# Optimization experiments

Hardware: AMD Instinct MI355X
Metric: run time of the kernel (lower is better)

Reference implementation:

```python
import jax, jax.numpy as jnp
import numpy as np

B, T, C = 8, 2048, 1024
NEG_INF = -1e38


def setup_inputs() -> dict:
    key = jax.random.key(0)
    ks = jax.random.split(key, 10)
    s = 1.0 / np.sqrt(C)
    return {
        "x": jax.random.normal(ks[0], (B, T, C), jnp.float32),
        "Wk": jax.random.normal(ks[1], (C, C), jnp.float32) * s,
        "Wv": jax.random.normal(ks[2], (C, C), jnp.float32) * s,
        "Wr": jax.random.normal(ks[3], (C, C), jnp.float32) * s,
        "Wo": jax.random.normal(ks[4], (C, C), jnp.float32) * s,
        "time_decay": jax.random.normal(ks[5], (C,), jnp.float32) * 0.5,
        "time_first": jax.random.normal(ks[6], (C,), jnp.float32) * 0.5,
        "time_mix_key": jax.random.uniform(ks[7], (1, 1, C), jnp.float32),
        "time_mix_value": jax.random.uniform(ks[8], (1, 1, C), jnp.float32),
        "time_mix_receptance": jax.random.uniform(ks[9], (1, 1, C), jnp.float32),
    }


def _wkv(k, v, time_decay, time_first):
    # k, v: [B, T, C]; numerically-stabilized exp-sum recurrence over T
    w = -jnp.exp(time_decay)  # [C]
    u = time_first            # [C]

    def step(carry, kv):
        num, den, mx = carry
        kt, vt = kv  # [B, C]
        # output at this step uses u bonus
        m_out = jnp.maximum(mx, kt + u)
        e1 = jnp.exp(mx - m_out)
        e2 = jnp.exp(kt + u - m_out)
        out = (e1 * num + e2 * vt) / (e1 * den + e2)
        # state update with decay w
        m_new = jnp.maximum(mx + w, kt)
        e1 = jnp.exp(mx + w - m_new)
        e2 = jnp.exp(kt - m_new)
        return (e1 * num + e2 * vt, e1 * den + e2, m_new), out

    init = (jnp.zeros((B, C), jnp.float32),
            jnp.zeros((B, C), jnp.float32),
            jnp.full((B, C), NEG_INF, jnp.float32))
    kT = jnp.swapaxes(k, 0, 1)  # [T, B, C]
    vT = jnp.swapaxes(v, 0, 1)
    _, outs = jax.lax.scan(step, init, (kT, vT))
    return jnp.swapaxes(outs, 0, 1)  # [B, T, C]


def reference(x, Wk, Wv, Wr, Wo, time_decay, time_first,
              time_mix_key, time_mix_value, time_mix_receptance):
    # time_shift: prev_x[t] = x[t-1], zero at t=0
    prev_x = jnp.concatenate([jnp.zeros_like(x[:, :1]), x[:, :-1]], axis=1)

    r_in = x * time_mix_receptance + prev_x * (1 - time_mix_receptance)
    k_in = x * time_mix_key + prev_x * (1 - time_mix_key)
    v_in = x * time_mix_value + prev_x * (1 - time_mix_value)

    receptance = jnp.einsum('btc,dc->btd', r_in, Wr)
    key = jnp.einsum('btc,dc->btd', k_in, Wk)
    value = jnp.einsum('btc,dc->btd', v_in, Wv)

    wkv = _wkv(key, value, time_decay, time_first)
    rwkv = jax.nn.sigmoid(receptance) * wkv
    return jnp.einsum('btc,dc->btd', rwkv, Wo)
```

## Files before the change

### kernel.cpp

```cpp
#include <hip/hip_runtime.h>
#include <cstdint>
#include <cstddef>

#define DEVI __device__ __forceinline__

typedef __attribute__((ext_vector_type(8))) short short8;
typedef __attribute__((ext_vector_type(4))) float f32x4;

constexpr int Bc = 8, Tc = 2048, Cc = 1024;
constexpr int WKV_L = 32, WKV_NCH = 64;

DEVI unsigned short f2b(float f) {
  unsigned int u = __float_as_uint(f);
  unsigned int r = (u + 0x7FFFu + ((u >> 16) & 1u)) >> 16;
  return (unsigned short)r;
}
DEVI float b2f(unsigned short u) {
  return __uint_as_float(((unsigned int)u) << 16);
}

DEVI void gload16(const unsigned short* g, unsigned short* l) {
  __builtin_amdgcn_global_load_lds(
      (const __attribute__((address_space(1))) void*)g,
      (__attribute__((address_space(3))) void*)l, 16, 0, 0);
}

__global__ void convert_bf16_kernel(const float* __restrict__ in,
                                    unsigned short* __restrict__ out, int n4) {
  int i = blockIdx.x * blockDim.x + threadIdx.x;
  if (i >= n4) return;
  const float4 v = ((const float4*)in)[i];
  ushort4 o;
  o.x = f2b(v.x); o.y = f2b(v.y); o.z = f2b(v.z); o.w = f2b(v.w);
  ((ushort4*)out)[i] = o;
}

__global__ void mix3_kernel(const float* __restrict__ x,
                            const float* __restrict__ tmk,
                            const float* __restrict__ tmv,
                            const float* __restrict__ tmr,
                            unsigned short* __restrict__ kin,
                            unsigned short* __restrict__ vin,
                            unsigned short* __restrict__ rin,
                            long n4) {
  long i = (long)blockIdx.x * blockDim.x + threadIdx.x;
  const long stride = (long)gridDim.x * blockDim.x;
  for (; i < n4; i += stride) {
    const long e = i * 4;
    const int c = (int)(e & (Cc - 1));
    const long bt = e >> 10;
    const int t = (int)(bt & (Tc - 1));
    const float4 xv = *(const float4*)(x + e);
    float4 pv = {0.f, 0.f, 0.f, 0.f};
    if (t > 0) pv = *(const float4*)(x + e - Cc);
    const float4 mk = *(const float4*)(tmk + c);
    const float4 mv = *(const float4*)(tmv + c);
    const float4 mr = *(const float4*)(tmr + c);
    const float* xp = (const float*)&xv;
    const float* pp = (const float*)&pv;
    const float* mkp = (const float*)&mk;
    const float* mvp = (const float*)&mv;
    const float* mrp = (const float*)&mr;
    ushort4 ko, vo, ro;
    unsigned short* kop = (unsigned short*)&ko;
    unsigned short* vop = (unsigned short*)&vo;
    unsigned short* rop = (unsigned short*)&ro;
#pragma unroll
    for (int q = 0; q < 4; ++q) {
      kop[q] = f2b(xp[q] * mkp[q] + pp[q] * (1.f - mkp[q]));
      vop[q] = f2b(xp[q] * mvp[q] + pp[q] * (1.f - mvp[q]));
      rop[q] = f2b(xp[q] * mrp[q] + pp[q] * (1.f - mrp[q]));
    }
    *(ushort4*)(kin + e) = ko;
    *(ushort4*)(vin + e) = vo;
    *(ushort4*)(rin + e) = ro;
  }
}

template <typename OutT>
__global__ __launch_bounds__(512, 2)
void gemm256(const unsigned short* __restrict__ A0,
             const unsigned short* __restrict__ W0, OutT* __restrict__ C0,
             const unsigned short* __restrict__ A1,
             const unsigned short* __restrict__ W1, OutT* __restrict__ C1,
             const unsigned short* __restrict__ A2,
             const unsigned short* __restrict__ W2, OutT* __restrict__ C2,
             int K, int N) {
  constexpr int BK = 64;
  __shared__ alignas(16) unsigned short As[2][256 * BK];
  __shared__ alignas(16) unsigned short Bs[2][256 * BK];
  const int z = blockIdx.z;
  const unsigned short* A = z == 0 ? A0 : (z == 1 ? A1 : A2);
  const unsigned short* W = z == 0 ? W0 : (z == 1 ? W1 : W2);
  OutT* C_out = z == 0 ? C0 : (z == 1 ? C1 : C2);
  const int m0 = blockIdx.x * 256;
  const int n0 = blockIdx.y * 256;
  const int tid = threadIdx.x;
  const int lane = tid & 63;
  const int w = tid >> 6;
  const int wm = w >> 2;
  const int wn = w & 3;
  const int fr = lane & 15;
  const int ksl = lane >> 4;

  f32x4 acc[8][4];
#pragma unroll
  for (int i = 0; i < 8; ++i)
#pragma unroll
    for (int j = 0; j < 4; ++j) acc[i][j] = (f32x4){0.f, 0.f, 0.f, 0.f};

#define STAGE(buf, kt)                                                        \
  {                                                                           \
    _Pragma("unroll")                                                         \
    for (int cc = 0; cc < 4; ++cc) {                                          \
      const int c = w * 256 + cc * 64 + lane;                                 \
      const int row = c >> 3;                                                 \
      const int gsl = (c & 7) ^ (row & 7);                                    \
      gload16(A + (size_t)(m0 + row) * K + (kt) + gsl * 8,                    \
              &As[buf][(w * 256 + cc * 64) * 8]);                             \
      gload16(W + (size_t)(n0 + row) * K + (kt) + gsl * 8,                    \
              &Bs[buf][(w * 256 + cc * 64) * 8]);                             \
    }                                                                         \
  }

  const int nt = K / BK;
  STAGE(0, 0);
  int cur = 0;
  for (int t = 0; t < nt; ++t) {
    asm volatile("s_waitcnt vmcnt(0)" ::: "memory");
    __builtin_amdgcn_s_barrier();
    asm volatile("" ::: "memory");
    if (t + 1 < nt) STAGE(cur ^ 1, (t + 1) * BK);
#pragma unroll
    for (int ks = 0; ks < 2; ++ks) {
      const int sl = ks * 4 + ksl;
      short8 af[8], bf[4];
#pragma unroll
      for (int i = 0; i < 8; ++i) {
        const int row = wm * 128 + i * 16 + fr;
        af[i] = *(const short8*)&As[cur][row * 64 + ((sl ^ (row & 7)) * 8)];
      }
#pragma unroll
      for (int j = 0; j < 4; ++j) {
        const int row = wn * 64 + j * 16 + fr;
        bf[j] = *(const short8*)&Bs[cur][row * 64 + ((sl ^ (row & 7)) * 8)];
      }
      __builtin_amdgcn_s_setprio(1);
#pragma unroll
      for (int i = 0; i < 8; ++i)
#pragma unroll
        for (int j = 0; j < 4; ++j)
          acc[i][j] = __builtin_amdgcn_mfma_f32_16x16x32_bf16(af[i], bf[j],
                                                              acc[i][j], 0, 0, 0);
      __builtin_amdgcn_s_setprio(0);
    }
    asm volatile("" ::: "memory");
    cur ^= 1;
  }
#undef STAGE

  const int orow = (lane >> 4) * 4;
  const int ocol = lane & 15;
#pragma unroll
  for (int i = 0; i < 8; ++i)
#pragma unroll
    for (int j = 0; j < 4; ++j) {
      const size_t rbase = (size_t)(m0 + wm * 128 + i * 16 + orow);
      const int cb = n0 + wn * 64 + j * 16 + ocol;
#pragma unroll
      for (int q = 0; q < 4; ++q) {
        const float vq = acc[i][j][q];
        if constexpr (sizeof(OutT) == 2)
          C_out[(rbase + q) * N + cb] = (OutT)f2b(vq);
        else
          C_out[(rbase + q) * N + cb] = (OutT)vq;
      }
    }
}

__global__ void wkv_phase1(const unsigned short* __restrict__ keyb,
                           const unsigned short* __restrict__ valb,
                           const float* __restrict__ td,
                           float* __restrict__ s_num,
                           float* __restrict__ s_den,
                           float* __restrict__ s_mx) {
  const int g = blockIdx.x * blockDim.x + threadIdx.x;
  const int c = g & (Cc - 1);
  const int j = (g / Cc) & (WKV_NCH - 1);
  const int b = g / (Cc * WKV_NCH);
  const float w = -__expf(td[c]);
  float num = 0.f, den = 0.f, mx = -1e38f;
  size_t idx = ((size_t)b * Tc + (size_t)j * WKV_L) * Cc + c;
#pragma unroll 4
  for (int i = 0; i < WKV_L; ++i, idx += Cc) {
    const float kt = b2f(keyb[idx]);
    const float vt = b2f(valb[idx]);
    const float mw = mx + w;
    const float mn = fmaxf(mw, kt);
    const float a1 = __expf(mw - mn);
    const float a2 = __expf(kt - mn);
    num = a1 * num + a2 * vt;
    den = a1 * den + a2;
    mx = mn;
  }
  s_num[g] = num; s_den[g] = den; s_mx[g] = mx;
}

__global__ void wkv_phase2(const float* __restrict__ td,
                           float* __restrict__ s_num,
                           float* __restrict__ s_den,
                           float* __restrict__ s_mx) {
  const int g = blockIdx.x * blockDim.x + threadIdx.x;
  const int c = g & (Cc - 1);
  const int b = g / Cc;
  const float Lw = -__expf(td[c]) * (float)WKV_L;
  float num = 0.f, den = 0.f, mx = -1e38f;
  size_t base = (size_t)b * WKV_NCH * Cc + c;
  for (int j = 0; j < WKV_NCH; ++j) {
    const size_t s = base + (size_t)j * Cc;
    const float ln = s_num[s], ld = s_den[s], lm = s_mx[s];
    s_num[s] = num; s_den[s] = den; s_mx[s] = mx;
    const float md = mx + Lw;
    const float m = fmaxf(md, lm);
    const float e1 = __expf(md - m);
    const float e2 = __expf(lm - m);
    num = e1 * num + e2 * ln;
    den = e1 * den + e2 * ld;
    mx = m;
  }
}

__global__ void wkv_phase3(const unsigned short* __restrict__ keyb,
                           const unsigned short* __restrict__ valb,
                           const unsigned short* __restrict__ recb,
                           const float* __restrict__ td,
                           const float* __restrict__ tf,
                           const float* __restrict__ s_num,
                           const float* __restrict__ s_den,
                           const float* __restrict__ s_mx,
                           unsigned short* __restrict__ rwkv) {
  const int g = blockIdx.x * blockDim.x + threadIdx.x;
  const int c = g & (Cc - 1);
  const int j = (g / Cc) & (WKV_NCH - 1);
  const int b = g / (Cc * WKV_NCH);
  const float w = -__expf(td[c]);
  const float u = tf[c];
  float num = s_num[g], den = s_den[g], mx = s_mx[g];
  size_t idx = ((size_t)b * Tc + (size_t)j * WKV_L) * Cc + c;
#pragma unroll 2
  for (int i = 0; i < WKV_L; ++i, idx += Cc) {
    const float kt = b2f(keyb[idx]);
    const float vt = b2f(valb[idx]);
    const float rt = b2f(recb[idx]);
    const float ku = kt + u;
    const float mo = fmaxf(mx, ku);
    const float e1 = __expf(mx - mo);
    const float e2 = __expf(ku - mo);
    const float out = (e1 * num + e2 * vt) / (e1 * den + e2);
    const float sr = 1.f / (1.f + __expf(-rt));
    rwkv[idx] = f2b(sr * out);
    const float mw = mx + w;
    const float mn = fmaxf(mw, kt);
    const float a1 = __expf(mw - mn);
    const float a2 = __expf(kt - mn);
    num = a1 * num + a2 * vt;
    den = a1 * den + a2;
    mx = mn;
  }
}

extern "C" void kernel_launch(void* const* d_in, const int* in_sizes, int n_in,
                              void* d_out, int out_size, void* d_ws, size_t ws_size,
                              hipStream_t stream) {
  const float* x   = (const float*)d_in[0];
  const float* Wk  = (const float*)d_in[1];
  const float* Wv  = (const float*)d_in[2];
  const float* Wr  = (const float*)d_in[3];
  const float* Wo  = (const float*)d_in[4];
  const float* td  = (const float*)d_in[5];
  const float* tf  = (const float*)d_in[6];
  const float* tmk = (const float*)d_in[7];
  const float* tmv = (const float*)d_in[8];
  const float* tmr = (const float*)d_in[9];

  const long BT = (long)Bc * Tc;
  const long NE = BT * Cc;
  const long CC = (long)Cc * Cc;

  char* p = (char*)d_ws;
  unsigned short* Wk_b = (unsigned short*)p; p += CC * 2;
  unsigned short* Wv_b = (unsigned short*)p; p += CC * 2;
  unsigned short* Wr_b = (unsigned short*)p; p += CC * 2;
  unsigned short* Wo_b = (unsigned short*)p; p += CC * 2;
  unsigned short* kin  = (unsigned short*)p; p += NE * 2;
  unsigned short* vin  = (unsigned short*)p; p += NE * 2;
  unsigned short* rin  = (unsigned short*)p; p += NE * 2;
  unsigned short* keyb = (unsigned short*)p; p += NE * 2;
  unsigned short* valb = (unsigned short*)p; p += NE * 2;
  unsigned short* recb = (unsigned short*)p; p += NE * 2;
  unsigned short* rwkv = kin;
  const long NS = (long)Bc * WKV_NCH * Cc;
  float* s_num = (float*)vin;
  float* s_den = s_num + NS;
  float* s_mx  = s_den + NS;

  {
    const int n4 = (int)(CC / 4);
    dim3 g((n4 + 255) / 256), b_(256);
    convert_bf16_kernel<<<g, b_, 0, stream>>>(Wk, Wk_b, n4);
    convert_bf16_kernel<<<g, b_, 0, stream>>>(Wv, Wv_b, n4);
    convert_bf16_kernel<<<g, b_, 0, stream>>>(Wr, Wr_b, n4);
    convert_bf16_kernel<<<g, b_, 0, stream>>>(Wo, Wo_b, n4);
  }

  mix3_kernel<<<2048, 256, 0, stream>>>(x, tmk, tmv, tmr, kin, vin, rin, NE / 4);

  {
    dim3 grid((unsigned)(BT / 256), (unsigned)(Cc / 256), 3), blk(512);
    gemm256<unsigned short><<<grid, blk, 0, stream>>>(
        kin, Wk_b, keyb, vin, Wv_b, valb, rin, Wr_b, recb, Cc, Cc);
  }

  wkv_phase1<<<2048, 256, 0, stream>>>(keyb, valb, td, s_num, s_den, s_mx);
  wkv_phase2<<<32, 256, 0, stream>>>(td, s_num, s_den, s_mx);
  wkv_phase3<<<2048, 256, 0, stream>>>(keyb, valb, recb, td, tf,
                                       s_num, s_den, s_mx, rwkv);

  {
    dim3 grid((unsigned)(BT / 256), (unsigned)(Cc / 256), 1), blk(512);
    gemm256<float><<<grid, blk, 0, stream>>>(
        rwkv, Wo_b, (float*)d_out, rwkv, Wo_b, (float*)d_out,
        rwkv, Wo_b, (float*)d_out, Cc, Cc);
  }
}
```

Measured before the change: 266.9 us.

## Ping-pong schedule GEMM with barrier-split LDS reads and MFMA phases plus tile swizzle

Restructures the GEMM main loop into four phases that alternate LDS fragment reads and 16-MFMA bursts, separated by workgroup barriers. The goal is to overlap the two waves per SIMD, so one issues LDS reads while the other runs MFMA, and to hide the global prefetch until the final phase. It also remaps block indices so groups of M tiles that share an N tile run close together, for better L2 reuse. The extra barriers add synchronisation overhead and could serialise work if the two waves fall out of phase.

```diff
diff --git a/kernel.cpp b/kernel.cpp
--- a/kernel.cpp
+++ b/kernel.cpp
@@ -77,15 +77,17 @@
   }
 }
 
+#define FENCE() asm volatile("" ::: "memory")
+
 template <typename OutT>
 __global__ __launch_bounds__(512, 2)
-void gemm256(const unsigned short* __restrict__ A0,
-             const unsigned short* __restrict__ W0, OutT* __restrict__ C0,
-             const unsigned short* __restrict__ A1,
-             const unsigned short* __restrict__ W1, OutT* __restrict__ C1,
-             const unsigned short* __restrict__ A2,
-             const unsigned short* __restrict__ W2, OutT* __restrict__ C2,
-             int K, int N) {
+void gemm256p(const unsigned short* __restrict__ A0,
+              const unsigned short* __restrict__ W0, OutT* __restrict__ C0,
+              const unsigned short* __restrict__ A1,
+              const unsigned short* __restrict__ W1, OutT* __restrict__ C1,
+              const unsigned short* __restrict__ A2,
+              const unsigned short* __restrict__ W2, OutT* __restrict__ C2,
+              int K, int N) {
   constexpr int BK = 64;
   __shared__ alignas(16) unsigned short As[2][256 * BK];
   __shared__ alignas(16) unsigned short Bs[2][256 * BK];
@@ -93,8 +95,11 @@
   const unsigned short* A = z == 0 ? A0 : (z == 1 ? A1 : A2);
   const unsigned short* W = z == 0 ? W0 : (z == 1 ? W1 : W2);
   OutT* C_out = z == 0 ? C0 : (z == 1 ? C1 : C2);
-  const int m0 = blockIdx.x * 256;
-  const int n0 = blockIdx.y * 256;
+  const int h = (int)blockIdx.x + ((int)blockIdx.y << 6);
+  const int m_idx = ((h & 7) << 3) | ((h >> 3) & 7);
+  const int n_idx = h >> 6;
+  const int m0 = m_idx * 256;
+  const int n0 = n_idx * 256;
   const int tid = threadIdx.x;
   const int lane = tid & 63;
   const int w = tid >> 6;
@@ -113,9 +118,9 @@
   {                                                                           \
     _Pragma("unroll")                                                         \
     for (int cc = 0; cc < 4; ++cc) {                                          \
-      const int c = w * 256 + cc * 64 + lane;                                 \
-      const int row = c >> 3;                                                 \
-      const int gsl = (c & 7) ^ (row & 7);                                    \
+      const int cch = w * 256 + cc * 64 + lane;                               \
+      const int row = cch >> 3;                                               \
+      const int gsl = (cch & 7) ^ (row & 7);                                  \
       gload16(A + (size_t)(m0 + row) * K + (kt) + gsl * 8,                    \
               &As[buf][(w * 256 + cc * 64) * 8]);                             \
       gload16(W + (size_t)(n0 + row) * K + (kt) + gsl * 8,                    \
@@ -123,41 +128,72 @@
     }                                                                         \
   }
 
+#define LDSRD(bufp, row, sl) \
+  (*(const short8*)&(bufp)[(row) * 64 + (((sl) ^ ((row) & 7)) * 8)])
+
+#define MFMA16(ar, bi)                                                        \
+  {                                                                           \
+    __builtin_amdgcn_s_setprio(1);                                            \
+    _Pragma("unroll")                                                         \
+    for (int i = 0; i < 4; ++i)                                               \
+      _Pragma("unroll")                                                       \
+      for (int j = 0; j < 4; ++j)                                             \
+        acc[(bi) + i][j] = __builtin_amdgcn_mfma_f32_16x16x32_bf16(           \
+            ar[i], bf[j], acc[(bi) + i][j], 0, 0, 0);                         \
+    __builtin_amdgcn_s_setprio(0);                                            \
+  }
+
+#define BAR() { FENCE(); __builtin_amdgcn_s_barrier(); FENCE(); }
+
   const int nt = K / BK;
   STAGE(0, 0);
+  asm volatile("s_waitcnt vmcnt(0)" ::: "memory");
+  BAR();
   int cur = 0;
   for (int t = 0; t < nt; ++t) {
-    asm volatile("s_waitcnt vmcnt(0)" ::: "memory");
-    __builtin_amdgcn_s_barrier();
-    asm volatile("" ::: "memory");
+    const unsigned short* Ab = As[cur];
+    const unsigned short* Bb = Bs[cur];
+    const int sl0 = ksl;
+    const int sl1 = 4 + ksl;
+    short8 af[4], bf[4];
+#pragma unroll
+    for (int i = 0; i < 4; ++i)
+      af[i] = LDSRD(Ab, wm * 128 + i * 16 + fr, sl0);
+#pragma unroll
+    for (int j = 0; j < 4; ++j)
+      bf[j] = LDSRD(Bb, wn * 64 + j * 16 + fr, sl0);
     if (t + 1 < nt) STAGE(cur ^ 1, (t + 1) * BK);
-#pragma unroll
-    for (int ks = 0; ks < 2; ++ks) {
-      const int sl = ks * 4 + ksl;
-      short8 af[8], bf[4];
-#pragma unroll
-      for (int i = 0; i < 8; ++i) {
-        const int row = wm * 128 + i * 16 + fr;
-        af[i] = *(const short8*)&As[cur][row * 64 + ((sl ^ (row & 7)) * 8)];
-      }
-#pragma unroll
-      for (int j = 0; j < 4; ++j) {
-        const int row = wn * 64 + j * 16 + fr;
-        bf[j] = *(const short8*)&Bs[cur][row * 64 + ((sl ^ (row & 7)) * 8)];
-      }
-      __builtin_amdgcn_s_setprio(1);
-#pragma unroll
-      for (int i = 0; i < 8; ++i)
-#pragma unroll
-        for (int j = 0; j < 4; ++j)
-          acc[i][j] = __builtin_amdgcn_mfma_f32_16x16x32_bf16(af[i], bf[j],
-                                                              acc[i][j], 0, 0, 0);
-      __builtin_amdgcn_s_setprio(0);
-    }
-    asm volatile("" ::: "memory");
+    BAR();
+    MFMA16(af, 0);
+    BAR();
+#pragma unroll
+    for (int i = 0; i < 4; ++i)
+      af[i] = LDSRD(Ab, wm * 128 + (4 + i) * 16 + fr, sl0);
+    BAR();
+    MFMA16(af, 4);
+    BAR();
+#pragma unroll
+    for (int i = 0; i < 4; ++i)
+      af[i] = LDSRD(Ab, wm * 128 + i * 16 + fr, sl1);
+#pragma unroll
+    for (int j = 0; j < 4; ++j)
+      bf[j] = LDSRD(Bb, wn * 64 + j * 16 + fr, sl1);
+    BAR();
+    MFMA16(af, 0);
+    BAR();
+#pragma unroll
+    for (int i = 0; i < 4; ++i)
+      af[i] = LDSRD(Ab, wm * 128 + (4 + i) * 16 + fr, sl1);
+    if (t + 1 < nt) asm volatile("s_waitcnt vmcnt(0)" ::: "memory");
+    BAR();
+    MFMA16(af, 4);
+    BAR();
     cur ^= 1;
   }
 #undef STAGE
+#undef LDSRD
+#undef MFMA16
+#undef BAR
 
   const int orow = (lane >> 4) * 4;
   const int ocol = lane & 15;
@@ -317,7 +353,7 @@
 
   {
     dim3 grid((unsigned)(BT / 256), (unsigned)(Cc / 256), 3), blk(512);
-    gemm256<unsigned short><<<grid, blk, 0, stream>>>(
+    gemm256p<unsigned short><<<grid, blk, 0, stream>>>(
         kin, Wk_b, keyb, vin, Wv_b, valb, rin, Wr_b, recb, Cc, Cc);
   }
 
@@ -328,7 +364,7 @@
 
   {
     dim3 grid((unsigned)(BT / 256), (unsigned)(Cc / 256), 1), blk(512);
-    gemm256<float><<<grid, blk, 0, stream>>>(
+    gemm256p<float><<<grid, blk, 0, stream>>>(
         rwkv, Wo_b, (float*)d_out, rwkv, Wo_b, (float*)d_out,
         rwkv, Wo_b, (float*)d_out, Cc, Cc);
   }
```

After: 270.6 us. Within noise of the previous version (+1.4%).

## Deepen GEMM pipeline to 4-stage BK=32 with block swizzle; fuse weight converts

Applied to the files above, without the earlier changes.

Reworks the bf16 GEMM mainloop from a double-buffered BK=64 scheme to a four-buffer BK=32 pipeline that keeps three tiles of loads in flight, using partial vmcnt waits and a new LDS XOR swizzle. It also remaps block indices so neighbouring blocks share weight tiles for better L2 reuse. The four weight conversion launches are merged into one. The intent is to hide global load latency and improve cache locality. The cost is twice as many barriers per K, and it relies on the hardcoded vmcnt counts and the 64-wide grid assumption being correct.

```diff
diff --git a/kernel.cpp b/kernel.cpp
--- a/kernel.cpp
+++ b/kernel.cpp
@@ -25,10 +25,20 @@
       (__attribute__((address_space(3))) void*)l, 16, 0, 0);
 }
 
-__global__ void convert_bf16_kernel(const float* __restrict__ in,
-                                    unsigned short* __restrict__ out, int n4) {
-  int i = blockIdx.x * blockDim.x + threadIdx.x;
-  if (i >= n4) return;
+#define FENCE() asm volatile("" ::: "memory")
+
+__global__ void convert4_kernel(const float* __restrict__ W0,
+                                const float* __restrict__ W1,
+                                const float* __restrict__ W2,
+                                const float* __restrict__ W3,
+                                unsigned short* __restrict__ o0,
+                                unsigned short* __restrict__ o1,
+                                unsigned short* __restrict__ o2,
+                                unsigned short* __restrict__ o3) {
+  const int i = blockIdx.x * blockDim.x + threadIdx.x;
+  const int s = blockIdx.y;
+  const float* in = s == 0 ? W0 : (s == 1 ? W1 : (s == 2 ? W2 : W3));
+  unsigned short* out = s == 0 ? o0 : (s == 1 ? o1 : (s == 2 ? o2 : o3));
   const float4 v = ((const float4*)in)[i];
   ushort4 o;
   o.x = f2b(v.x); o.y = f2b(v.y); o.z = f2b(v.z); o.w = f2b(v.w);
@@ -79,22 +89,25 @@
 
 template <typename OutT>
 __global__ __launch_bounds__(512, 2)
-void gemm256(const unsigned short* __restrict__ A0,
-             const unsigned short* __restrict__ W0, OutT* __restrict__ C0,
-             const unsigned short* __restrict__ A1,
-             const unsigned short* __restrict__ W1, OutT* __restrict__ C1,
-             const unsigned short* __restrict__ A2,
-             const unsigned short* __restrict__ W2, OutT* __restrict__ C2,
-             int K, int N) {
-  constexpr int BK = 64;
-  __shared__ alignas(16) unsigned short As[2][256 * BK];
-  __shared__ alignas(16) unsigned short Bs[2][256 * BK];
+void gemm256c(const unsigned short* __restrict__ A0,
+              const unsigned short* __restrict__ W0, OutT* __restrict__ C0,
+              const unsigned short* __restrict__ A1,
+              const unsigned short* __restrict__ W1, OutT* __restrict__ C1,
+              const unsigned short* __restrict__ A2,
+              const unsigned short* __restrict__ W2, OutT* __restrict__ C2,
+              int K, int N) {
+  constexpr int BK = 32;
+  __shared__ alignas(16) unsigned short As[4][256 * BK];
+  __shared__ alignas(16) unsigned short Bs[4][256 * BK];
   const int z = blockIdx.z;
   const unsigned short* A = z == 0 ? A0 : (z == 1 ? A1 : A2);
   const unsigned short* W = z == 0 ? W0 : (z == 1 ? W1 : W2);
   OutT* C_out = z == 0 ? C0 : (z == 1 ? C1 : C2);
-  const int m0 = blockIdx.x * 256;
-  const int n0 = blockIdx.y * 256;
+  const int h = (int)blockIdx.x + ((int)blockIdx.y << 6);
+  const int m_idx = ((h & 7) << 3) | ((h >> 3) & 7);
+  const int n_idx = h >> 6;
+  const int m0 = m_idx * 256;
+  const int n0 = n_idx * 256;
   const int tid = threadIdx.x;
   const int lane = tid & 63;
   const int w = tid >> 6;
@@ -112,52 +125,53 @@
 #define STAGE(buf, kt)                                                        \
   {                                                                           \
     _Pragma("unroll")                                                         \
-    for (int cc = 0; cc < 4; ++cc) {                                          \
-      const int c = w * 256 + cc * 64 + lane;                                 \
-      const int row = c >> 3;                                                 \
-      const int gsl = (c & 7) ^ (row & 7);                                    \
+    for (int cc = 0; cc < 2; ++cc) {                                          \
+      const int c = w * 128 + cc * 64 + lane;                                 \
+      const int row = c >> 2;                                                 \
+      const int gsl = (c & 3) ^ ((row >> 1) & 3);                             \
       gload16(A + (size_t)(m0 + row) * K + (kt) + gsl * 8,                    \
-              &As[buf][(w * 256 + cc * 64) * 8]);                             \
+              &As[buf][(size_t)c * 8]);                                       \
       gload16(W + (size_t)(n0 + row) * K + (kt) + gsl * 8,                    \
-              &Bs[buf][(w * 256 + cc * 64) * 8]);                             \
+              &Bs[buf][(size_t)c * 8]);                                       \
     }                                                                         \
   }
+
+#define LDSRD(bufp, row, sl) \
+  (*(const short8*)&(bufp)[(row) * 32 + ((((sl) ^ (((row) >> 1) & 3))) * 8)])
 
   const int nt = K / BK;
   STAGE(0, 0);
-  int cur = 0;
+  STAGE(1, BK);
+  STAGE(2, 2 * BK);
   for (int t = 0; t < nt; ++t) {
-    asm volatile("s_waitcnt vmcnt(0)" ::: "memory");
+    const int rem = nt - t;
+    if (rem > 2)       asm volatile("s_waitcnt vmcnt(8)" ::: "memory");
+    else if (rem == 2) asm volatile("s_waitcnt vmcnt(4)" ::: "memory");
+    else               asm volatile("s_waitcnt vmcnt(0)" ::: "memory");
     __builtin_amdgcn_s_barrier();
-    asm volatile("" ::: "memory");
-    if (t + 1 < nt) STAGE(cur ^ 1, (t + 1) * BK);
-#pragma unroll
-    for (int ks = 0; ks < 2; ++ks) {
-      const int sl = ks * 4 + ksl;
-      short8 af[8], bf[4];
-#pragma unroll
-      for (int i = 0; i < 8; ++i) {
-        const int row = wm * 128 + i * 16 + fr;
-        af[i] = *(const short8*)&As[cur][row * 64 + ((sl ^ (row & 7)) * 8)];
-      }
-#pragma unroll
-      for (int j = 0; j < 4; ++j) {
-        const int row = wn * 64 + j * 16 + fr;
-        bf[j] = *(const short8*)&Bs[cur][row * 64 + ((sl ^ (row & 7)) * 8)];
-      }
-      __builtin_amdgcn_s_setprio(1);
-#pragma unroll
-      for (int i = 0; i < 8; ++i)
-#pragma unroll
-        for (int j = 0; j < 4; ++j)
-          acc[i][j] = __builtin_amdgcn_mfma_f32_16x16x32_bf16(af[i], bf[j],
-                                                              acc[i][j], 0, 0, 0);
-      __builtin_amdgcn_s_setprio(0);
-    }
-    asm volatile("" ::: "memory");
-    cur ^= 1;
+    FENCE();
+    if (t + 3 < nt) STAGE((t + 3) & 3, (t + 3) * BK);
+    const unsigned short* Ab = As[t & 3];
+    const unsigned short* Bb = Bs[t & 3];
+    short8 af[8], bf[4];
+#pragma unroll
+    for (int i = 0; i < 8; ++i)
+      af[i] = LDSRD(Ab, wm * 128 + i * 16 + fr, ksl);
+#pragma unroll
+    for (int j = 0; j < 4; ++j)
+      bf[j] = LDSRD(Bb, wn * 64 + j * 16 + fr, ksl);
+    __builtin_amdgcn_s_setprio(1);
+#pragma unroll
+    for (int i = 0; i < 8; ++i)
+#pragma unroll
+      for (int j = 0; j < 4; ++j)
+        acc[i][j] = __builtin_amdgcn_mfma_f32_16x16x32_bf16(af[i], bf[j],
+                                                            acc[i][j], 0, 0, 0);
+    __builtin_amdgcn_s_setprio(0);
+    FENCE();
   }
 #undef STAGE
+#undef LDSRD
 
   const int orow = (lane >> 4) * 4;
   const int ocol = lane & 15;
@@ -305,19 +319,16 @@
   float* s_mx  = s_den + NS;
 
   {
-    const int n4 = (int)(CC / 4);
-    dim3 g((n4 + 255) / 256), b_(256);
-    convert_bf16_kernel<<<g, b_, 0, stream>>>(Wk, Wk_b, n4);
-    convert_bf16_kernel<<<g, b_, 0, stream>>>(Wv, Wv_b, n4);
-    convert_bf16_kernel<<<g, b_, 0, stream>>>(Wr, Wr_b, n4);
-    convert_bf16_kernel<<<g, b_, 0, stream>>>(Wo, Wo_b, n4);
+    dim3 g((unsigned)(CC / 4 / 256), 4), b_(256);
+    convert4_kernel<<<g, b_, 0, stream>>>(Wk, Wv, Wr, Wo,
+                                          Wk_b, Wv_b, Wr_b, Wo_b);
   }
 
   mix3_kernel<<<2048, 256, 0, stream>>>(x, tmk, tmv, tmr, kin, vin, rin, NE / 4);
 
   {
     dim3 grid((unsigned)(BT / 256), (unsigned)(Cc / 256), 3), blk(512);
-    gemm256<unsigned short><<<grid, blk, 0, stream>>>(
+    gemm256c<unsigned short><<<grid, blk, 0, stream>>>(
         kin, Wk_b, keyb, vin, Wv_b, valb, rin, Wr_b, recb, Cc, Cc);
   }
 
@@ -328,7 +339,7 @@
 
   {
     dim3 grid((unsigned)(BT / 256), (unsigned)(Cc / 256), 1), blk(512);
-    gemm256<float><<<grid, blk, 0, stream>>>(
+    gemm256c<float><<<grid, blk, 0, stream>>>(
         rwkv, Wo_b, (float*)d_out, rwkv, Wo_b, (float*)d_out,
         rwkv, Wo_b, (float*)d_out, Cc, Cc);
   }
```

After: 282.4 us. +5.8%, slower.
